# Performance work log

Measured on AMD Instinct MI355X. Metric: run time of the kernel, lower is better.

Reference implementation:

```python
import jax, jax.numpy as jnp
import numpy as np

B, C, T = 8, 256, 2048
REDUCED = max(C // 8, 8)  # 32


def setup_inputs() -> dict:
    key = jax.random.key(0)
    ks = jax.random.split(key, 7)
    s = 1.0 / np.sqrt(C)
    return {
        "x": jax.random.normal(ks[0], (B, C, T), dtype=jnp.float32),
        "Wq": jax.random.uniform(ks[1], (REDUCED, C), jnp.float32, -s, s),
        "bq": jax.random.uniform(ks[2], (REDUCED,), jnp.float32, -s, s),
        "Wk": jax.random.uniform(ks[3], (REDUCED, C), jnp.float32, -s, s),
        "bk": jax.random.uniform(ks[4], (REDUCED,), jnp.float32, -s, s),
        "Wv": jax.random.uniform(ks[5], (C, C), jnp.float32, -s, s),
        "bv": jax.random.uniform(ks[6], (C,), jnp.float32, -s, s),
        "gamma": jnp.zeros((1,), dtype=jnp.float32) + 0.1,  # nonzero so output depends on attention
    }


def reference(x, Wq, bq, Wk, bk, Wv, bv, gamma):
    # conv1x1 projections == per-timestep linear over channels
    q = jnp.einsum("rc,bct->btr", Wq, x) + bq            # [B, T, reduced]
    k = jnp.einsum("rc,bct->brt", Wk, x) + bk[:, None]   # [B, reduced, T]
    v = jnp.einsum("oc,bct->bto", Wv, x) + bv            # [B, T, C]
    attn = jnp.einsum("btr,brs->bts", q, k)              # [B, T, T]
    attn = jax.nn.softmax(attn, axis=-1)
    out = jnp.einsum("bts,bsc->btc", attn, v)            # [B, T, C]
    out = jnp.transpose(out, (0, 2, 1))                  # [B, C, T]
    return x + gamma * out
```

## Files before the change

kernel.cpp:

```cpp
#include <hip/hip_runtime.h>
#include <hip/hip_bf16.h>
#include <math.h>

constexpr int BB = 8;
constexpr int CC = 256;
constexpr int TT = 2048;
constexpr int RR = 32;

constexpr int VS = 72;
constexpr int PS = 72;

constexpr int XS32 = 65;
constexpr int XSB  = 264;

constexpr float FIXEDM = 24.0f;

typedef short short8 __attribute__((ext_vector_type(8)));
typedef float f32x4 __attribute__((ext_vector_type(4)));
typedef unsigned short us4 __attribute__((ext_vector_type(4)));

static __device__ __forceinline__ unsigned short f2bf(float f) {
    __hip_bfloat16 h = __float2bfloat16(f);
    return *reinterpret_cast<unsigned short*>(&h);
}

__global__ __launch_bounds__(256) void proj_kernel(
    const float* __restrict__ x,
    const float* __restrict__ Wq, const float* __restrict__ bq,
    const float* __restrict__ Wk, const float* __restrict__ bk,
    const float* __restrict__ Wv, const float* __restrict__ bv,
    unsigned short* __restrict__ qws, unsigned short* __restrict__ kws,
    unsigned short* __restrict__ vws)
{
    __shared__ float xs32[64 * XS32];
    __shared__ unsigned short xsb[64 * XSB];

    const int tid = threadIdx.x;
    const int t0  = blockIdx.x * 64;
    const int b   = blockIdx.y;
    const float* xb = x + (size_t)b * CC * TT;

    for (int p = 0; p < 4; ++p) {
        #pragma unroll
        for (int m = 0; m < 4; ++m) {
            int lin = m * 256 + tid;
            int cl  = lin >> 4;
            int t4  = lin & 15;
            float4 v = *(const float4*)(xb + (size_t)(p * 64 + cl) * TT + t0 + t4 * 4);
            float* d = &xs32[cl * XS32 + t4 * 4];
            d[0] = v.x; d[1] = v.y; d[2] = v.z; d[3] = v.w;
        }
        __syncthreads();
        {
            int wv = tid >> 6, cl = tid & 63;
            #pragma unroll
            for (int j = 0; j < 16; ++j) {
                int t = j * 4 + wv;
                xsb[t * XSB + p * 64 + cl] = f2bf(xs32[cl * XS32 + t]);
            }
        }
        __syncthreads();
    }

    const int lane = tid & 63;
    const int w    = __builtin_amdgcn_readfirstlane(tid >> 6);
    const int l15  = lane & 15;
    const int quad = lane >> 4;

    const float* Wt[5]; const float* bt[5]; int rl[5]; int seg[5];
    #pragma unroll
    for (int i = 0; i < 5; ++i) {
        int mt = w * 5 + i;
        if (mt < 2)      { Wt[i] = Wq; bt[i] = bq; rl[i] = mt * 16;       seg[i] = 0; }
        else if (mt < 4) { Wt[i] = Wk; bt[i] = bk; rl[i] = (mt - 2) * 16; seg[i] = 1; }
        else             { Wt[i] = Wv; bt[i] = bv; rl[i] = (mt - 4) * 16; seg[i] = 2; }
    }

    f32x4 acc[5][4];
    #pragma unroll
    for (int i = 0; i < 5; ++i) {
        float4 bb = *(const float4*)(bt[i] + rl[i] + quad * 4);
        #pragma unroll
        for (int nt = 0; nt < 4; ++nt)
            acc[i][nt] = (f32x4){bb.x, bb.y, bb.z, bb.w};
    }

    #pragma unroll
    for (int ks = 0; ks < 8; ++ks) {
        short8 bfr[4];
        #pragma unroll
        for (int nt = 0; nt < 4; ++nt)
            bfr[nt] = *(const short8*)(&xsb[(nt * 16 + l15) * XSB + ks * 32 + quad * 8]);
        #pragma unroll
        for (int i = 0; i < 5; ++i) {
            const float* wp = Wt[i] + (size_t)(rl[i] + l15) * CC + ks * 32 + quad * 8;
            float4 a0 = *(const float4*)wp;
            float4 a1 = *(const float4*)(wp + 4);
            short8 af;
            af[0] = (short)f2bf(a0.x); af[1] = (short)f2bf(a0.y);
            af[2] = (short)f2bf(a0.z); af[3] = (short)f2bf(a0.w);
            af[4] = (short)f2bf(a1.x); af[5] = (short)f2bf(a1.y);
            af[6] = (short)f2bf(a1.z); af[7] = (short)f2bf(a1.w);
            #pragma unroll
            for (int nt = 0; nt < 4; ++nt)
                acc[i][nt] = __builtin_amdgcn_mfma_f32_16x16x32_bf16(
                    af, bfr[nt], acc[i][nt], 0, 0, 0);
        }
    }

    #pragma unroll
    for (int i = 0; i < 5; ++i) {
        if (seg[i] < 2) {
            unsigned short* outt = (seg[i] == 0 ? qws : kws) + (size_t)b * TT * RR;
            #pragma unroll
            for (int nt = 0; nt < 4; ++nt) {
                int t = t0 + nt * 16 + l15;
                us4 pk;
                pk[0] = f2bf(acc[i][nt][0]); pk[1] = f2bf(acc[i][nt][1]);
                pk[2] = f2bf(acc[i][nt][2]); pk[3] = f2bf(acc[i][nt][3]);
                *(us4*)(outt + (size_t)t * RR + rl[i] + quad * 4) = pk;
            }
        } else {
            unsigned short* vt = vws + (size_t)b * CC * TT;
            #pragma unroll
            for (int nt = 0; nt < 4; ++nt)
                #pragma unroll
                for (int r = 0; r < 4; ++r)
                    vt[(size_t)(rl[i] + quad * 4 + r) * TT + t0 + nt * 16 + l15] =
                        f2bf(acc[i][nt][r]);
        }
    }
}

__global__ __launch_bounds__(256, 1) void attn_kernel(
    const float* __restrict__ x,
    const unsigned short* __restrict__ qws, const unsigned short* __restrict__ kws,
    const unsigned short* __restrict__ vws, const float* __restrict__ gamma_p,
    float* __restrict__ out)
{
    __shared__ unsigned short Vs[CC * VS];
    __shared__ unsigned short Ps[64 * PS];
    __shared__ float linv_s[64];

    const int tid  = threadIdx.x;
    const int b    = blockIdx.x;
    const int t0   = blockIdx.y * 64;
    const int lane = tid & 63;
    const int w    = __builtin_amdgcn_readfirstlane(tid >> 6);
    const int l15  = lane & 15;
    const int quad = lane >> 4;

    const unsigned short* qb = qws + (size_t)b * TT * RR;
    const unsigned short* kb = kws + (size_t)b * TT * RR;
    const unsigned short* vb = vws + (size_t)b * CC * TT;

    short8 qfrag = *(const short8*)(qb + (size_t)(t0 + w * 16 + l15) * RR + quad * 8);

    float rs[4];
    #pragma unroll
    for (int r = 0; r < 4; ++r) rs[r] = 0.0f;

    f32x4 acc[4][4];
    #pragma unroll
    for (int mt = 0; mt < 4; ++mt)
        #pragma unroll
        for (int nt = 0; nt < 4; ++nt)
            acc[mt][nt] = (f32x4){0.f, 0.f, 0.f, 0.f};

    const f32x4 zz = (f32x4){0.f, 0.f, 0.f, 0.f};

    for (int s0 = 0; s0 < TT; s0 += 64) {
        __syncthreads();

        #pragma unroll
        for (int m = 0; m < 8; ++m) {
            int lin = m * 256 + tid;
            int c   = lin >> 3;
            int s8  = lin & 7;
            short8 v8 = *(const short8*)(vb + (size_t)c * TT + s0 + s8 * 8);
            *(short8*)(&Vs[c * VS + s8 * 8]) = v8;
        }

        f32x4 st[4];
        #pragma unroll
        for (int nt = 0; nt < 4; ++nt) {
            short8 kf = *(const short8*)(kb + (size_t)(s0 + nt * 16 + l15) * RR + quad * 8);
            st[nt] = __builtin_amdgcn_mfma_f32_16x16x32_bf16(qfrag, kf, zz, 0, 0, 0);
        }

        const int prow = w * 16 + quad * 4;
        #pragma unroll
        for (int nt = 0; nt < 4; ++nt) {
            #pragma unroll
            for (int r = 0; r < 4; ++r) {
                float e = __expf(st[nt][r] - FIXEDM);
                rs[r] += e;
                Ps[(prow + r) * PS + nt * 16 + l15] = f2bf(e);
            }
        }
        __syncthreads();

        #pragma unroll
        for (int ks = 0; ks < 2; ++ks) {
            short8 pa[4], vf[4];
            #pragma unroll
            for (int mt = 0; mt < 4; ++mt)
                pa[mt] = *(const short8*)(&Ps[(mt * 16 + l15) * PS + ks * 32 + quad * 8]);
            #pragma unroll
            for (int nt = 0; nt < 4; ++nt)
                vf[nt] = *(const short8*)(&Vs[(w * 64 + nt * 16 + l15) * VS + ks * 32 + quad * 8]);
            #pragma unroll
            for (int mt = 0; mt < 4; ++mt)
                #pragma unroll
                for (int nt = 0; nt < 4; ++nt)
                    acc[mt][nt] = __builtin_amdgcn_mfma_f32_16x16x32_bf16(
                        pa[mt], vf[nt], acc[mt][nt], 0, 0, 0);
        }
    }

    #pragma unroll
    for (int mask = 1; mask < 16; mask <<= 1)
        #pragma unroll
        for (int r = 0; r < 4; ++r)
            rs[r] += __shfl_xor(rs[r], mask, 64);
    if (l15 == 0) {
        #pragma unroll
        for (int r = 0; r < 4; ++r)
            linv_s[w * 16 + quad * 4 + r] = 1.0f / rs[r];
    }
    __syncthreads();

    const float gam = gamma_p[0];
    const float* xb = x + (size_t)b * CC * TT;
    float* ob = out + (size_t)b * CC * TT;

    #pragma unroll
    for (int mt = 0; mt < 4; ++mt) {
        f32x4 li4 = *(const f32x4*)(&linv_s[mt * 16 + quad * 4]);
        #pragma unroll
        for (int nt = 0; nt < 4; ++nt) {
            int c = w * 64 + nt * 16 + l15;
            size_t g = (size_t)c * TT + t0 + mt * 16 + quad * 4;
            float4 xv = *(const float4*)(xb + g);
            float4 ov;
            ov.x = xv.x + gam * acc[mt][nt][0] * li4[0];
            ov.y = xv.y + gam * acc[mt][nt][1] * li4[1];
            ov.z = xv.z + gam * acc[mt][nt][2] * li4[2];
            ov.w = xv.w + gam * acc[mt][nt][3] * li4[3];
            *(float4*)(ob + g) = ov;
        }
    }
}

extern "C" void kernel_launch(void* const* d_in, const int* in_sizes, int n_in,
                              void* d_out, int out_size, void* d_ws, size_t ws_size,
                              hipStream_t stream)
{
    const float* x     = (const float*)d_in[0];
    const float* Wq    = (const float*)d_in[1];
    const float* bq    = (const float*)d_in[2];
    const float* Wk    = (const float*)d_in[3];
    const float* bk    = (const float*)d_in[4];
    const float* Wv    = (const float*)d_in[5];
    const float* bv    = (const float*)d_in[6];
    const float* gamma = (const float*)d_in[7];
    float* out = (float*)d_out;

    unsigned short* qws = (unsigned short*)d_ws;
    unsigned short* kws = qws + (size_t)BB * TT * RR;
    unsigned short* vws = kws + (size_t)BB * TT * RR;

    dim3 pgrid(TT / 64, BB);
    proj_kernel<<<pgrid, 256, 0, stream>>>(x, Wq, bq, Wk, bk, Wv, bv, qws, kws, vws);

    dim3 agrid(BB, TT / 64);
    attn_kernel<<<agrid, 256, 0, stream>>>(x, qws, kws, vws, gamma, out);
}
```

Baseline: 156.6 us.

## Split attention key range across two wave groups with register-prefetched K/V tiles

The attention kernel now runs 512 threads as two groups of four waves. Each group handles alternate 64-key tiles with its own V and P shared buffers, and the two partial outputs and row sums are reduced through shared memory at the end. The next K/V tile is prefetched into registers while the current PV MFMAs run, to hide global load latency. The projection kernel switches to 32-timestep tiles with a single staging pass and two blocks per CU, raising block count. The cost is more registers and shared memory per block, plus an extra reduction and synchronisation step.

```diff
diff --git a/kernel.cpp b/kernel.cpp
--- a/kernel.cpp
+++ b/kernel.cpp
@@ -9,8 +9,10 @@
 
 constexpr int VS = 72;
 constexpr int PS = 72;
-
-constexpr int XS32 = 65;
+constexpr int OSTR = 68;
+
+constexpr int PT  = 32;
+constexpr int XS32 = 33;
 constexpr int XSB  = 264;
 
 constexpr float FIXEDM = 24.0f;
@@ -24,7 +26,7 @@
     return *reinterpret_cast<unsigned short*>(&h);
 }
 
-__global__ __launch_bounds__(256) void proj_kernel(
+__global__ __launch_bounds__(256, 2) void proj_kernel(
     const float* __restrict__ x,
     const float* __restrict__ Wq, const float* __restrict__ bq,
     const float* __restrict__ Wk, const float* __restrict__ bk,
@@ -32,35 +34,31 @@
     unsigned short* __restrict__ qws, unsigned short* __restrict__ kws,
     unsigned short* __restrict__ vws)
 {
-    __shared__ float xs32[64 * XS32];
-    __shared__ unsigned short xsb[64 * XSB];
+    __shared__ float xs32[CC * XS32];
+    __shared__ unsigned short xsb[PT * XSB];
 
     const int tid = threadIdx.x;
-    const int t0  = blockIdx.x * 64;
+    const int t0  = blockIdx.x * PT;
     const int b   = blockIdx.y;
     const float* xb = x + (size_t)b * CC * TT;
 
-    for (int p = 0; p < 4; ++p) {
-        #pragma unroll
-        for (int m = 0; m < 4; ++m) {
-            int lin = m * 256 + tid;
-            int cl  = lin >> 4;
-            int t4  = lin & 15;
-            float4 v = *(const float4*)(xb + (size_t)(p * 64 + cl) * TT + t0 + t4 * 4);
-            float* d = &xs32[cl * XS32 + t4 * 4];
-            d[0] = v.x; d[1] = v.y; d[2] = v.z; d[3] = v.w;
-        }
-        __syncthreads();
-        {
-            int wv = tid >> 6, cl = tid & 63;
-            #pragma unroll
-            for (int j = 0; j < 16; ++j) {
-                int t = j * 4 + wv;
-                xsb[t * XSB + p * 64 + cl] = f2bf(xs32[cl * XS32 + t]);
-            }
-        }
-        __syncthreads();
-    }
+    #pragma unroll
+    for (int m = 0; m < 8; ++m) {
+        int lin = m * 256 + tid;
+        int c   = lin >> 3;
+        int t4  = lin & 7;
+        float4 v = *(const float4*)(xb + (size_t)c * TT + t0 + t4 * 4);
+        float* d = &xs32[c * XS32 + t4 * 4];
+        d[0] = v.x; d[1] = v.y; d[2] = v.z; d[3] = v.w;
+    }
+    __syncthreads();
+    {
+        int c = tid;
+        #pragma unroll
+        for (int t = 0; t < PT; ++t)
+            xsb[t * XSB + c] = f2bf(xs32[c * XS32 + t]);
+    }
+    __syncthreads();
 
     const int lane = tid & 63;
     const int w    = __builtin_amdgcn_readfirstlane(tid >> 6);
@@ -76,20 +74,20 @@
         else             { Wt[i] = Wv; bt[i] = bv; rl[i] = (mt - 4) * 16; seg[i] = 2; }
     }
 
-    f32x4 acc[5][4];
+    f32x4 acc[5][2];
     #pragma unroll
     for (int i = 0; i < 5; ++i) {
         float4 bb = *(const float4*)(bt[i] + rl[i] + quad * 4);
         #pragma unroll
-        for (int nt = 0; nt < 4; ++nt)
+        for (int nt = 0; nt < 2; ++nt)
             acc[i][nt] = (f32x4){bb.x, bb.y, bb.z, bb.w};
     }
 
     #pragma unroll
     for (int ks = 0; ks < 8; ++ks) {
-        short8 bfr[4];
-        #pragma unroll
-        for (int nt = 0; nt < 4; ++nt)
+        short8 bfr[2];
+        #pragma unroll
+        for (int nt = 0; nt < 2; ++nt)
             bfr[nt] = *(const short8*)(&xsb[(nt * 16 + l15) * XSB + ks * 32 + quad * 8]);
         #pragma unroll
         for (int i = 0; i < 5; ++i) {
@@ -102,7 +100,7 @@
             af[4] = (short)f2bf(a1.x); af[5] = (short)f2bf(a1.y);
             af[6] = (short)f2bf(a1.z); af[7] = (short)f2bf(a1.w);
             #pragma unroll
-            for (int nt = 0; nt < 4; ++nt)
+            for (int nt = 0; nt < 2; ++nt)
                 acc[i][nt] = __builtin_amdgcn_mfma_f32_16x16x32_bf16(
                     af, bfr[nt], acc[i][nt], 0, 0, 0);
         }
@@ -113,7 +111,7 @@
         if (seg[i] < 2) {
             unsigned short* outt = (seg[i] == 0 ? qws : kws) + (size_t)b * TT * RR;
             #pragma unroll
-            for (int nt = 0; nt < 4; ++nt) {
+            for (int nt = 0; nt < 2; ++nt) {
                 int t = t0 + nt * 16 + l15;
                 us4 pk;
                 pk[0] = f2bf(acc[i][nt][0]); pk[1] = f2bf(acc[i][nt][1]);
@@ -123,7 +121,7 @@
         } else {
             unsigned short* vt = vws + (size_t)b * CC * TT;
             #pragma unroll
-            for (int nt = 0; nt < 4; ++nt)
+            for (int nt = 0; nt < 2; ++nt)
                 #pragma unroll
                 for (int r = 0; r < 4; ++r)
                     vt[(size_t)(rl[i] + quad * 4 + r) * TT + t0 + nt * 16 + l15] =
@@ -132,14 +130,14 @@
     }
 }
 
-__global__ __launch_bounds__(256, 1) void attn_kernel(
+__global__ __launch_bounds__(512, 2) void attn_kernel(
     const float* __restrict__ x,
     const unsigned short* __restrict__ qws, const unsigned short* __restrict__ kws,
     const unsigned short* __restrict__ vws, const float* __restrict__ gamma_p,
     float* __restrict__ out)
 {
-    __shared__ unsigned short Vs[CC * VS];
-    __shared__ unsigned short Ps[64 * PS];
+    __shared__ __align__(16) unsigned short smem[2 * CC * VS + 2 * 64 * PS];
+    __shared__ float lsum[64];
     __shared__ float linv_s[64];
 
     const int tid  = threadIdx.x;
@@ -147,14 +145,20 @@
     const int t0   = blockIdx.y * 64;
     const int lane = tid & 63;
     const int w    = __builtin_amdgcn_readfirstlane(tid >> 6);
+    const int g    = w >> 2;
+    const int w0   = w & 3;
     const int l15  = lane & 15;
     const int quad = lane >> 4;
+    const int tl   = tid & 255;
+
+    unsigned short* Vs = smem + g * (CC * VS);
+    unsigned short* Ps = smem + 2 * (CC * VS) + g * (64 * PS);
 
     const unsigned short* qb = qws + (size_t)b * TT * RR;
     const unsigned short* kb = kws + (size_t)b * TT * RR;
     const unsigned short* vb = vws + (size_t)b * CC * TT;
 
-    short8 qfrag = *(const short8*)(qb + (size_t)(t0 + w * 16 + l15) * RR + quad * 8);
+    short8 qfrag = *(const short8*)(qb + (size_t)(t0 + w0 * 16 + l15) * RR + quad * 8);
 
     float rs[4];
     #pragma unroll
@@ -169,26 +173,38 @@
 
     const f32x4 zz = (f32x4){0.f, 0.f, 0.f, 0.f};
 
-    for (int s0 = 0; s0 < TT; s0 += 64) {
-        __syncthreads();
-
+    short8 vreg[8], kreg[4];
+    {
+        int s0 = g * 64;
         #pragma unroll
         for (int m = 0; m < 8; ++m) {
-            int lin = m * 256 + tid;
+            int lin = m * 256 + tl;
             int c   = lin >> 3;
             int s8  = lin & 7;
-            short8 v8 = *(const short8*)(vb + (size_t)c * TT + s0 + s8 * 8);
-            *(short8*)(&Vs[c * VS + s8 * 8]) = v8;
+            vreg[m] = *(const short8*)(vb + (size_t)c * TT + s0 + s8 * 8);
+        }
+        #pragma unroll
+        for (int nt = 0; nt < 4; ++nt)
+            kreg[nt] = *(const short8*)(kb + (size_t)(s0 + nt * 16 + l15) * RR + quad * 8);
+    }
+
+    for (int j = 0; j < 16; ++j) {
+        __syncthreads();
+
+        #pragma unroll
+        for (int m = 0; m < 8; ++m) {
+            int lin = m * 256 + tl;
+            int c   = lin >> 3;
+            int s8  = lin & 7;
+            *(short8*)(&Vs[c * VS + s8 * 8]) = vreg[m];
         }
 
         f32x4 st[4];
         #pragma unroll
-        for (int nt = 0; nt < 4; ++nt) {
-            short8 kf = *(const short8*)(kb + (size_t)(s0 + nt * 16 + l15) * RR + quad * 8);
-            st[nt] = __builtin_amdgcn_mfma_f32_16x16x32_bf16(qfrag, kf, zz, 0, 0, 0);
-        }
-
-        const int prow = w * 16 + quad * 4;
+        for (int nt = 0; nt < 4; ++nt)
+            st[nt] = __builtin_amdgcn_mfma_f32_16x16x32_bf16(qfrag, kreg[nt], zz, 0, 0, 0);
+
+        const int prow = w0 * 16 + quad * 4;
         #pragma unroll
         for (int nt = 0; nt < 4; ++nt) {
             #pragma unroll
@@ -200,6 +216,20 @@
         }
         __syncthreads();
 
+        if (j < 15) {
+            int s1 = (j + 1) * 128 + g * 64;
+            #pragma unroll
+            for (int m = 0; m < 8; ++m) {
+                int lin = m * 256 + tl;
+                int c   = lin >> 3;
+                int s8  = lin & 7;
+                vreg[m] = *(const short8*)(vb + (size_t)c * TT + s1 + s8 * 8);
+            }
+            #pragma unroll
+            for (int nt = 0; nt < 4; ++nt)
+                kreg[nt] = *(const short8*)(kb + (size_t)(s1 + nt * 16 + l15) * RR + quad * 8);
+        }
+
         #pragma unroll
         for (int ks = 0; ks < 2; ++ks) {
             short8 pa[4], vf[4];
@@ -208,7 +238,7 @@
                 pa[mt] = *(const short8*)(&Ps[(mt * 16 + l15) * PS + ks * 32 + quad * 8]);
             #pragma unroll
             for (int nt = 0; nt < 4; ++nt)
-                vf[nt] = *(const short8*)(&Vs[(w * 64 + nt * 16 + l15) * VS + ks * 32 + quad * 8]);
+                vf[nt] = *(const short8*)(&Vs[(w0 * 64 + nt * 16 + l15) * VS + ks * 32 + quad * 8]);
             #pragma unroll
             for (int mt = 0; mt < 4; ++mt)
                 #pragma unroll
@@ -223,31 +253,60 @@
         #pragma unroll
         for (int r = 0; r < 4; ++r)
             rs[r] += __shfl_xor(rs[r], mask, 64);
-    if (l15 == 0) {
-        #pragma unroll
-        for (int r = 0; r < 4; ++r)
-            linv_s[w * 16 + quad * 4 + r] = 1.0f / rs[r];
-    }
+
     __syncthreads();
 
-    const float gam = gamma_p[0];
-    const float* xb = x + (size_t)b * CC * TT;
-    float* ob = out + (size_t)b * CC * TT;
-
-    #pragma unroll
-    for (int mt = 0; mt < 4; ++mt) {
-        f32x4 li4 = *(const f32x4*)(&linv_s[mt * 16 + quad * 4]);
-        #pragma unroll
-        for (int nt = 0; nt < 4; ++nt) {
-            int c = w * 64 + nt * 16 + l15;
-            size_t g = (size_t)c * TT + t0 + mt * 16 + quad * 4;
-            float4 xv = *(const float4*)(xb + g);
-            float4 ov;
-            ov.x = xv.x + gam * acc[mt][nt][0] * li4[0];
-            ov.y = xv.y + gam * acc[mt][nt][1] * li4[1];
-            ov.z = xv.z + gam * acc[mt][nt][2] * li4[2];
-            ov.w = xv.w + gam * acc[mt][nt][3] * li4[3];
-            *(float4*)(ob + g) = ov;
+    float* scratch = (float*)smem;
+    if (g == 1) {
+        #pragma unroll
+        for (int mt = 0; mt < 4; ++mt)
+            #pragma unroll
+            for (int nt = 0; nt < 4; ++nt)
+                *(f32x4*)(&scratch[(w0 * 64 + nt * 16 + l15) * OSTR + mt * 16 + quad * 4]) =
+                    acc[mt][nt];
+        if (l15 == 0) {
+            #pragma unroll
+            for (int r = 0; r < 4; ++r) lsum[w0 * 16 + quad * 4 + r] = rs[r];
+        }
+    }
+    __syncthreads();
+
+    if (g == 0) {
+        #pragma unroll
+        for (int mt = 0; mt < 4; ++mt)
+            #pragma unroll
+            for (int nt = 0; nt < 4; ++nt) {
+                f32x4 o = *(const f32x4*)(&scratch[(w0 * 64 + nt * 16 + l15) * OSTR + mt * 16 + quad * 4]);
+                acc[mt][nt][0] += o[0]; acc[mt][nt][1] += o[1];
+                acc[mt][nt][2] += o[2]; acc[mt][nt][3] += o[3];
+            }
+        #pragma unroll
+        for (int r = 0; r < 4; ++r) rs[r] += lsum[w0 * 16 + quad * 4 + r];
+        if (l15 == 0) {
+            #pragma unroll
+            for (int r = 0; r < 4; ++r)
+                linv_s[w0 * 16 + quad * 4 + r] = 1.0f / rs[r];
+        }
+
+        const float gam = gamma_p[0];
+        const float* xb = x + (size_t)b * CC * TT;
+        float* ob = out + (size_t)b * CC * TT;
+
+        #pragma unroll
+        for (int mt = 0; mt < 4; ++mt) {
+            f32x4 li4 = *(const f32x4*)(&linv_s[mt * 16 + quad * 4]);
+            #pragma unroll
+            for (int nt = 0; nt < 4; ++nt) {
+                int c = w0 * 64 + nt * 16 + l15;
+                size_t gidx = (size_t)c * TT + t0 + mt * 16 + quad * 4;
+                float4 xv = *(const float4*)(xb + gidx);
+                float4 ov;
+                ov.x = xv.x + gam * acc[mt][nt][0] * li4[0];
+                ov.y = xv.y + gam * acc[mt][nt][1] * li4[1];
+                ov.z = xv.z + gam * acc[mt][nt][2] * li4[2];
+                ov.w = xv.w + gam * acc[mt][nt][3] * li4[3];
+                *(float4*)(ob + gidx) = ov;
+            }
         }
     }
 }
@@ -270,9 +329,9 @@
     unsigned short* kws = qws + (size_t)BB * TT * RR;
     unsigned short* vws = kws + (size_t)BB * TT * RR;
 
-    dim3 pgrid(TT / 64, BB);
+    dim3 pgrid(TT / PT, BB);
     proj_kernel<<<pgrid, 256, 0, stream>>>(x, Wq, bq, Wk, bk, Wv, bv, qws, kws, vws);
 
     dim3 agrid(BB, TT / 64);
-    attn_kernel<<<agrid, 256, 0, stream>>>(x, qws, kws, vws, gamma, out);
+    attn_kernel<<<agrid, 512, 0, stream>>>(x, qws, kws, vws, gamma, out);
 }
```

New measurement: 149.6 us. -4.5%, faster.
